# Kernel optimization log

Measured on AMD Instinct MI355X. Metric: run time of the kernel, lower is better.

## Reference

```python
import jax, jax.numpy as jnp
import numpy as np

N, E, G, F = 50000, 800000, 64, 128
R_MAX = 5.0
P_CUT = 6.0
NUM_BESSEL = 8


def sph_harm(u):
    # component-normalized real spherical harmonics up to l=3 on unit vectors u [E,3]
    x, y, z = u[:, 0], u[:, 1], u[:, 2]
    one = jnp.ones_like(x)
    s3, s5, s15 = np.sqrt(3.0), np.sqrt(5.0), np.sqrt(15.0)
    c1, c2, c3 = np.sqrt(35.0 / 8.0), np.sqrt(105.0), np.sqrt(21.0 / 8.0)
    c4, c5 = np.sqrt(7.0) / 2.0, np.sqrt(105.0) / 2.0
    x2, y2, z2 = x * x, y * y, z * z
    comps = [
        one,
        s3 * x, s3 * y, s3 * z,
        s15 * x * y, s15 * y * z, 0.5 * s5 * (3.0 * z2 - 1.0), s15 * x * z, 0.5 * s15 * (x2 - y2),
        c1 * y * (3.0 * x2 - y2), c2 * x * y * z, c3 * y * (5.0 * z2 - 1.0),
        c4 * z * (5.0 * z2 - 3.0), c3 * x * (5.0 * z2 - 1.0), c5 * z * (x2 - y2),
        c1 * x * (x2 - 3.0 * y2),
    ]
    return jnp.stack(comps, axis=-1)  # [E,16]


def radial_embedding(r):
    # Bessel basis with polynomial cutoff envelope; r [E]
    n = jnp.arange(1, NUM_BESSEL + 1, dtype=r.dtype)
    bessel = np.sqrt(2.0 / R_MAX) * jnp.sin(n * jnp.pi * r[:, None] / R_MAX) / r[:, None]
    u = r / R_MAX
    p = P_CUT
    env = (1.0 - (p + 1.0) * (p + 2.0) / 2.0 * u ** p
           + p * (p + 2.0) * u ** (p + 1.0)
           - p * (p + 1.0) / 2.0 * u ** (p + 2.0))
    env = env * (r < R_MAX).astype(r.dtype)
    return bessel * env[:, None]  # [E,8]


def setup_inputs() -> dict:
    key = jax.random.key(0)
    ks = jax.random.split(key, 12)
    return {
        "positions": jax.random.normal(ks[0], (N, 3), dtype=jnp.float32),
        "node_attrs": jax.random.uniform(ks[1], (N, 10), dtype=jnp.float32),
        "shifts": jnp.zeros((E, 3), dtype=jnp.float32),
        "edge_index": jax.random.randint(ks[2], (2, E), 0, N),
        "batch": jnp.sort(jax.random.randint(ks[3], (N,), 0, G)),
        "num_graphs": G,
        "W_emb": 0.1 * jax.random.normal(ks[4], (10, F), dtype=jnp.float32),
        "atomic_energies_t": jax.random.normal(ks[5], (10,), dtype=jnp.float32),
        "W_r": 0.1 * jax.random.normal(ks[6], (2, NUM_BESSEL, F), dtype=jnp.float32),
        "w_sh": 0.1 * jax.random.normal(ks[7], (2, 16), dtype=jnp.float32),
        "W_out": 0.1 * jax.random.normal(ks[8], (2, F, F), dtype=jnp.float32),
        "W_skip": 0.1 * jax.random.normal(ks[9], (2, 10, F), dtype=jnp.float32),
        "w_read": 0.1 * jax.random.normal(ks[10], (2, F), dtype=jnp.float32),
    }


def reference(positions, node_attrs, shifts, edge_index, batch, num_graphs,
              W_emb, atomic_energies_t, W_r, w_sh, W_out, W_skip, w_read):
    snd, rcv = edge_index[0], edge_index[1]

    def energy_fn(pos):
        vec = pos[rcv] - pos[snd] + shifts                      # [E,3] edge gather
        r = jnp.sqrt(jnp.sum(vec * vec, axis=-1) + 1e-12)       # [E]
        Y = sph_harm(vec / r[:, None])                          # [E,16]
        eb = radial_embedding(r)                                # [E,8]
        h = node_attrs @ W_emb                                  # [N,F] node embedding
        e0 = jax.ops.segment_sum(node_attrs @ atomic_energies_t, batch, num_segments=num_graphs)
        energy = e0
        for i in range(W_r.shape[0]):                           # interaction layers
            R = eb @ W_r[i]                                     # [E,F] radial weights
            s = Y @ w_sh[i]                                     # [E] angular weight
            m = h[snd] * R * s[:, None]                         # [E,F] messages
            agg = jax.ops.segment_sum(m, rcv, num_segments=pos.shape[0])  # [N,F]
            h = agg @ W_out[i] + node_attrs @ W_skip[i]
            node_e = h @ w_read[i]                              # [N] readout
            energy = energy + jax.ops.segment_sum(node_e, batch, num_segments=num_graphs)
        return energy                                           # [G]

    energy = energy_fn(positions)
    forces = -jax.grad(lambda p: energy_fn(p).sum())(positions)
    return energy, forces
```

## Files before the change

kernel.cpp:

```cpp
#include <hip/hip_runtime.h>

#define NN 50000
#define EE 800000
#define GG 64
#define FF 128
#define NBES 8
#define RECW 8
#define RMAXF 5.0f
#define PI_F 3.14159265358979323846f
#define NB ((NN + 255) / 256)

#define S3  1.7320508075688772f
#define S5  2.23606797749979f
#define S15 3.872983346207417f
#define C1c 2.091650066335189f
#define C2c 10.246950765959598f
#define C3c 1.62018517460196f
#define C4c 1.3228756555322954f
#define C5c 5.123475382979799f
#define CCB 0.6324555320336759f

__device__ __forceinline__ float shc_s(float x, float y, float z, const float* __restrict__ w) {
    float x2 = x * x, y2 = y * y, z2 = z * z;
    return w[0]
        + w[1] * (S3 * x) + w[2] * (S3 * y) + w[3] * (S3 * z)
        + w[4] * (S15 * x * y) + w[5] * (S15 * y * z) + w[6] * (0.5f * S5 * (3.f * z2 - 1.f))
        + w[7] * (S15 * x * z) + w[8] * (0.5f * S15 * (x2 - y2))
        + w[9] * (C1c * y * (3.f * x2 - y2)) + w[10] * (C2c * x * y * z)
        + w[11] * (C3c * y * (5.f * z2 - 1.f)) + w[12] * (C4c * z * (5.f * z2 - 3.f))
        + w[13] * (C3c * x * (5.f * z2 - 1.f)) + w[14] * (C5c * z * (x2 - y2))
        + w[15] * (C1c * x * (x2 - 3.f * y2));
}

__device__ __forceinline__ void shc_grad(float x, float y, float z, const float* __restrict__ w,
                                         float& gx, float& gy, float& gz) {
    float x2 = x * x, y2 = y * y, z2 = z * z;
    gx = w[1] * S3 + w[4] * (S15 * y) + w[7] * (S15 * z) + w[8] * (S15 * x)
       + w[9] * (6.f * C1c * x * y) + w[10] * (C2c * y * z) + w[13] * (C3c * (5.f * z2 - 1.f))
       + w[14] * (2.f * C5c * x * z) + w[15] * (3.f * C1c * (x2 - y2));
    gy = w[2] * S3 + w[4] * (S15 * x) + w[5] * (S15 * z) - w[8] * (S15 * y)
       + w[9] * (3.f * C1c * (x2 - y2)) + w[10] * (C2c * x * z) + w[11] * (C3c * (5.f * z2 - 1.f))
       - w[14] * (2.f * C5c * y * z) - w[15] * (6.f * C1c * x * y);
    gz = w[3] * S3 + w[5] * (S15 * y) + w[6] * (3.f * S5 * z) + w[7] * (S15 * x)
       + w[10] * (C2c * x * y) + w[11] * (10.f * C3c * y * z) + w[12] * (C4c * (15.f * z2 - 3.f))
       + w[13] * (10.f * C3c * x * z) + w[14] * (C5c * (x2 - y2));
}


__global__ __launch_bounds__(256) void count_kernel(const int* __restrict__ ei,
                                                    int* __restrict__ cnt,
                                                    int* __restrict__ rank_r,
                                                    int* __restrict__ rank_s) {
    int e = blockIdx.x * 256 + threadIdx.x;
    if (e >= EE) return;
    rank_r[e] = atomicAdd(&cnt[ei[EE + e]], 1);
    rank_s[e] = atomicAdd(&cnt[NN + ei[e]], 1);
}

__global__ __launch_bounds__(256) void scan_partial(const int* __restrict__ cnt,
                                                    int* __restrict__ parts) {
    __shared__ int wsum[4];
    int b = blockIdx.x;
    int half = b / NB;
    int cb = b - half * NB;
    int i = cb * 256 + threadIdx.x;
    int v = (i < NN) ? cnt[(size_t)half * NN + i] : 0;
    int x = v;
#pragma unroll
    for (int o = 32; o > 0; o >>= 1) x += __shfl_xor(x, o);
    int lane = threadIdx.x & 63, wid = threadIdx.x >> 6;
    if (lane == 0) wsum[wid] = x;
    __syncthreads();
    if (threadIdx.x == 0) parts[b] = wsum[0] + wsum[1] + wsum[2] + wsum[3];
}

__global__ __launch_bounds__(256) void scan_parts(int* __restrict__ parts,
                                                  int* __restrict__ off) {
    __shared__ int wsum[4];
    __shared__ int carry_s;
    int lane = threadIdx.x & 63, wid = threadIdx.x >> 6;
    for (int h = 0; h < 2; h++) {
        if (threadIdx.x == 0) carry_s = 0;
        __syncthreads();
        for (int base = 0; base < NB; base += 256) {
            int i = base + threadIdx.x;
            int v = (i < NB) ? parts[h * NB + i] : 0;
            int x = v;
#pragma unroll
            for (int d = 1; d < 64; d <<= 1) {
                int y = __shfl_up(x, d);
                if (lane >= d) x += y;
            }
            if (lane == 63) wsum[wid] = x;
            __syncthreads();
            int pre = 0;
#pragma unroll
            for (int w = 0; w < 4; w++) if (w < wid) pre += wsum[w];
            int total = wsum[0] + wsum[1] + wsum[2] + wsum[3];
            int carry = carry_s;
            if (i < NB) parts[h * NB + i] = carry + pre + x - v;
            __syncthreads();
            if (threadIdx.x == 0) carry_s = carry + total;
            __syncthreads();
        }
        if (threadIdx.x == 0) off[(size_t)h * (NN + 1) + NN] = carry_s;
        __syncthreads();
    }
}

__global__ __launch_bounds__(256) void scan_apply(const int* __restrict__ cnt,
                                                  const int* __restrict__ parts,
                                                  int* __restrict__ off) {
    __shared__ int wsum[4];
    int b = blockIdx.x;
    int half = b / NB;
    int cb = b - half * NB;
    int i = cb * 256 + threadIdx.x;
    int v = (i < NN) ? cnt[(size_t)half * NN + i] : 0;
    int lane = threadIdx.x & 63, wid = threadIdx.x >> 6;
    int x = v;
#pragma unroll
    for (int d = 1; d < 64; d <<= 1) {
        int y = __shfl_up(x, d);
        if (lane >= d) x += y;
    }
    if (lane == 63) wsum[wid] = x;
    __syncthreads();
    int pre = 0;
#pragma unroll
    for (int w = 0; w < 4; w++) if (w < wid) pre += wsum[w];
    if (i < NN) off[(size_t)half * (NN + 1) + i] = parts[b] + pre + x - v;
}

__global__ __launch_bounds__(256) void fill_kernel(const int* __restrict__ ei,
                                                   const int* __restrict__ off,
                                                   const int* __restrict__ rank_r,
                                                   const int* __restrict__ rank_s,
                                                   int* __restrict__ jr,
                                                   int* __restrict__ psl_j) {
    int e = blockIdx.x * 256 + threadIdx.x;
    if (e >= EE) return;
    int snd = ei[e], rcv = ei[EE + e];
    int sr = off[rcv] + rank_r[e];
    int ss = off[(NN + 1) + snd] + rank_s[e];
    jr[e] = sr;
    psl_j[ss] = sr;
}


__global__ __launch_bounds__(256) void edge_geom(const float* __restrict__ pos,
                                                 const float* __restrict__ shifts,
                                                 const int* __restrict__ ei,
                                                 const float* __restrict__ wsh,
                                                 const int* __restrict__ jr,
                                                 float* __restrict__ rec) {
    int e = blockIdx.x * 256 + threadIdx.x;
    if (e >= EE) return;
    int snd = ei[e];
    int rcv = ei[EE + e];
    float vx = pos[rcv * 3 + 0] - pos[snd * 3 + 0] + shifts[e * 3 + 0];
    float vy = pos[rcv * 3 + 1] - pos[snd * 3 + 1] + shifts[e * 3 + 1];
    float vz = pos[rcv * 3 + 2] - pos[snd * 3 + 2] + shifts[e * 3 + 2];
    float r2 = vx * vx + vy * vy + vz * vz + 1e-12f;
    float r = sqrtf(r2);
    float inv_r = 1.0f / r;
    float x = vx * inv_r, y = vy * inv_r, z = vz * inv_r;

    float s0 = shc_s(x, y, z, wsh);
    float s1v = shc_s(x, y, z, wsh + 16);

    float* rc = rec + (size_t)jr[e] * RECW;
    *(float4*)&rc[0] = make_float4(x, y, z, inv_r);
    *(float4*)&rc[4] = make_float4(s0, s1v, __int_as_float(snd), __int_as_float(rcv));
}


__global__ __launch_bounds__(256) void e1_csr(const float* __restrict__ rec,
                                              const int* __restrict__ off_snd,
                                              const int* __restrict__ psl_j,
                                              float* __restrict__ E1) {
    int gid = blockIdx.x * 256 + threadIdx.x;
    int n = gid >> 3;
    int k_l = gid & 7;
    if (n >= NN) return;
    float kf = (float)(k_l + 1);
    int beg = off_snd[n], end = off_snd[n + 1];
    float acc = 0.f;
    for (int s = beg; s < end; s++) {
        int j = psl_j[s];
        const float* rc = rec + (size_t)j * RECW;
        float inv_r = rc[3];
        float s1v = rc[5];
        float r = 1.0f / inv_r;
        float u = r * (1.0f / RMAXF);
        float th = PI_F * u;
        float u2 = u * u, u3 = u2 * u, u6 = u3 * u3, u7 = u6 * u, u8 = u6 * u2;
        float valid = (r < RMAXF) ? 1.f : 0.f;
        float env = (1.f - 28.f * u6 + 48.f * u7 - 21.f * u8) * valid;
        float my = sinf(kf * th);
        acc += my * (CCB * inv_r * env * s1v);
    }
    E1[(size_t)n * 8 + k_l] = acc;
}


__global__ __launch_bounds__(128) void a1_kernel(const float* __restrict__ Wout1,
                                                 const float* __restrict__ wread1,
                                                 const float* __restrict__ Wskip1,
                                                 const float* __restrict__ ae,
                                                 float* __restrict__ a1,
                                                 float* __restrict__ askip) {
    int f = threadIdx.x;
    float s = 0.f;
    for (int k = 0; k < FF; k++) s += Wout1[f * FF + k] * wread1[k];
    a1[f] = s;
    if (f < 10) {
        float t = 0.f;
        for (int k = 0; k < FF; k++) t += Wskip1[f * FF + k] * wread1[k];
        askip[f] = t + ae[f];
    }
}

__global__ __launch_bounds__(128) void cd_kernel(const float* __restrict__ Wout0,
                                                 const float* __restrict__ wread0,
                                                 const float* __restrict__ a1,
                                                 const float* __restrict__ Wr1,
                                                 float* __restrict__ c0,
                                                 float* __restrict__ D) {
    int fp = threadIdx.x;
    float c = 0.f;
    float d[NBES];
#pragma unroll
    for (int k = 0; k < NBES; k++) d[k] = 0.f;
    for (int f = 0; f < FF; f++) {
        float w = Wout0[fp * FF + f];
        c += wread0[f] * w;
        float aw = a1[f] * w;
#pragma unroll
        for (int k = 0; k < NBES; k++) d[k] += aw * Wr1[k * FF + f];
    }
    c0[fp] = c;
#pragma unroll
    for (int k = 0; k < NBES; k++) D[k * FF + fp] = d[k];
}

__global__ __launch_bounds__(256) void gw_kernel(const float* __restrict__ W_emb,
                                                 const float* __restrict__ Wr0,
                                                 const float* __restrict__ Wout0,
                                                 float* __restrict__ GW) {
    int idx = blockIdx.x * 256 + threadIdx.x;
    if (idx >= 80 * FF) return;
    int fp = idx & 127;
    int p = idx >> 7;
    int a = p >> 3, k = p & 7;
    float s = 0.f;
    for (int f = 0; f < FF; f++)
        s += W_emb[a * FF + f] * Wr0[k * FF + f] * Wout0[f * FF + fp];
    GW[p * FF + fp] = s;
}

__global__ __launch_bounds__(256) void tmc_kernel(const float* __restrict__ D,
                                                  const float* __restrict__ c0,
                                                  const float* __restrict__ W_emb,
                                                  const float* __restrict__ Wr0,
                                                  float* __restrict__ T,
                                                  float* __restrict__ Mc) {
    for (int i = threadIdx.x; i < 720; i += 256) {
        if (i < 640) {
            int kp = i / 80;
            int p0 = i - kp * 80;
            int k = p0 / 10, a = p0 - k * 10;
            float s = 0.f;
            for (int f = 0; f < FF; f++)
                s += D[kp * FF + f] * W_emb[a * FF + f] * Wr0[k * FF + f];
            T[i] = s;
        } else {
            int p0 = i - 640;
            int k = p0 / 10, a = p0 - k * 10;
            float s = 0.f;
            for (int f = 0; f < FF; f++)
                s += c0[f] * W_emb[a * FF + f] * Wr0[k * FF + f];
            Mc[p0] = s;
        }
    }
}


#define P0_BLOCKS 2048
__global__ __launch_bounds__(256) void p0_kernel(const float* __restrict__ rec,
                                                 const int* __restrict__ off,
                                                 const float* __restrict__ attrs,
                                                 float* __restrict__ P0) {
    int wv = (blockIdx.x * 256 + threadIdx.x) >> 6;
    int lane = threadIdx.x & 63;
    int nwaves = P0_BLOCKS * 4;
    int a_lo = lane >> 3;
    int k_l = lane & 7;
    float kf = (float)(k_l + 1);

    for (int n = wv; n < NN; n += nwaves) {
        int beg = off[n], end = off[n + 1];
        float acc = 0.f, acc2 = 0.f;
        for (int j = beg; j < end; j++) {
            const float* rc = rec + (size_t)j * RECW;
            float inv_r = rc[3];
            float s0 = rc[4];
            int snd = __float_as_int(rc[6]);
            float r = 1.0f / inv_r;
            float u = r * (1.0f / RMAXF);
            float th = PI_F * u;
            float u2 = u * u, u3 = u2 * u, u6 = u3 * u3, u7 = u6 * u, u8 = u6 * u2;
            float valid = (r < RMAXF) ? 1.f : 0.f;
            float env = (1.f - 28.f * u6 + 48.f * u7 - 21.f * u8) * valid;
            float my = sinf(kf * th);
            float es = my * (CCB * inv_r * env) * s0;
            acc += attrs[snd * 10 + a_lo] * es;
            if (lane < 16) acc2 += attrs[snd * 10 + 8 + a_lo] * es;
        }
        P0[(size_t)n * 80 + lane] = acc;
        if (lane < 16) P0[(size_t)n * 80 + 64 + lane] = acc2;
    }
}


#define GEMM_BLOCKS 512
__global__ __launch_bounds__(256, 2) void h1_gemm(const float* __restrict__ P0,
                                                  const float* __restrict__ GW,
                                                  const float* __restrict__ attrs,
                                                  const float* __restrict__ Wskip,
                                                  const float* __restrict__ wread,
                                                  float* __restrict__ h1,
                                                  float* __restrict__ node_e) {
    __shared__ float sb[80][FF];
    __shared__ float sa[32][80];
    int t = threadIdx.x;
#pragma unroll
    for (int j = 0; j < 10; j++) {
        int flat4 = j * 256 + t;
        int row = flat4 >> 5;
        int col = (flat4 & 31) * 4;
        *(float4*)&sb[row][col] = *(const float4*)&GW[row * FF + col];
    }

    int g = t >> 5;
    int f0 = (t & 31) * 4;
    const int NTILES = (NN + 31) / 32;

    for (int tile = blockIdx.x; tile < NTILES; tile += GEMM_BLOCKS) {
        __syncthreads();
#pragma unroll
        for (int j = 0; j < 3; j++) {
            int flat4 = j * 256 + t;
            if (flat4 < 640) {
                int row = flat4 / 20;
                int col = (flat4 - row * 20) * 4;
                int n = tile * 32 + row;
                float4 v = make_float4(0.f, 0.f, 0.f, 0.f);
                if (n < NN) v = *(const float4*)&P0[(size_t)n * 80 + col];
                *(float4*)&sa[row][col] = v;
            }
        }
        __syncthreads();

        float acc[4][4];
#pragma unroll
        for (int i = 0; i < 4; i++)
#pragma unroll
            for (int j = 0; j < 4; j++) acc[i][j] = 0.f;

        for (int kk = 0; kk < 80; kk += 4) {
            float4 bv0 = *(const float4*)&sb[kk + 0][f0];
            float4 bv1 = *(const float4*)&sb[kk + 1][f0];
            float4 bv2 = *(const float4*)&sb[kk + 2][f0];
            float4 bv3 = *(const float4*)&sb[kk + 3][f0];
#pragma unroll
            for (int ni = 0; ni < 4; ni++) {
                float4 av = *(const float4*)&sa[g * 4 + ni][kk];
                acc[ni][0] += av.x * bv0.x + av.y * bv1.x + av.z * bv2.x + av.w * bv3.x;
                acc[ni][1] += av.x * bv0.y + av.y * bv1.y + av.z * bv2.y + av.w * bv3.y;
                acc[ni][2] += av.x * bv0.z + av.y * bv1.z + av.z * bv2.z + av.w * bv3.z;
                acc[ni][3] += av.x * bv0.w + av.y * bv1.w + av.z * bv2.w + av.w * bv3.w;
            }
        }

#pragma unroll
        for (int ni = 0; ni < 4; ni++) {
            int n = tile * 32 + g * 4 + ni;
            bool valid = (n < NN);
#pragma unroll
            for (int a = 0; a < 10; a++) {
                float att = valid ? attrs[n * 10 + a] : 0.f;
                float4 wk = *(const float4*)&Wskip[a * FF + f0];
                acc[ni][0] += att * wk.x;
                acc[ni][1] += att * wk.y;
                acc[ni][2] += att * wk.z;
                acc[ni][3] += att * wk.w;
            }
            if (valid) {
                float4 out;
                out.x = acc[ni][0]; out.y = acc[ni][1];
                out.z = acc[ni][2]; out.w = acc[ni][3];
                *(float4*)&h1[(size_t)n * FF + f0] = out;
            }
            float4 wv = *(const float4*)&wread[f0];
            float p = acc[ni][0] * wv.x + acc[ni][1] * wv.y
                    + acc[ni][2] * wv.z + acc[ni][3] * wv.w;
#pragma unroll
            for (int o = 16; o > 0; o >>= 1) p += __shfl_xor(p, o);
            if (valid && (t & 31) == 0) node_e[n] = p;
        }
    }
}


__global__ __launch_bounds__(256) void t1_kernel(const float* __restrict__ h1,
                                                 const float* __restrict__ a1,
                                                 const float* __restrict__ Wr1,
                                                 float* __restrict__ t1) {
    int w = threadIdx.x >> 6;
    int lane = threadIdx.x & 63;
    int n = blockIdx.x * 4 + w;
    if (n >= NN) return;
    int f0 = lane, f1 = lane + 64;
    float v0 = a1[f0] * h1[(size_t)n * FF + f0];
    float v1 = a1[f1] * h1[(size_t)n * FF + f1];
    float p[NBES];
#pragma unroll
    for (int k = 0; k < NBES; k++)
        p[k] = v0 * Wr1[k * FF + f0] + v1 * Wr1[k * FF + f1];
#pragma unroll
    for (int o = 32; o > 0; o >>= 1) {
#pragma unroll
        for (int k = 0; k < NBES; k++) p[k] += __shfl_xor(p[k], o);
    }
    if (lane == 0) {
        *(float4*)&t1[(size_t)n * 8]     = make_float4(p[0], p[1], p[2], p[3]);
        *(float4*)&t1[(size_t)n * 8 + 4] = make_float4(p[4], p[5], p[6], p[7]);
    }
}


__global__ __launch_bounds__(256) void m_kernel(const float* __restrict__ E1,
                                                const float* __restrict__ T,
                                                const float* __restrict__ Mc,
                                                float* __restrict__ M) {
    __shared__ float sT[720];
    int t = threadIdx.x;
    for (int i = t; i < 720; i += 256) sT[i] = (i < 640) ? T[i] : Mc[i - 640];
    __syncthreads();
    int n = blockIdx.x * 256 + t;
    if (n >= NN) return;
    float4 ea = *(const float4*)&E1[(size_t)n * 8];
    float4 eb = *(const float4*)&E1[(size_t)n * 8 + 4];
    float e1v[8] = {ea.x, ea.y, ea.z, ea.w, eb.x, eb.y, eb.z, eb.w};
#pragma unroll
    for (int c = 0; c < 20; c++) {
        float4 m = *(const float4*)&sT[640 + c * 4];
#pragma unroll
        for (int kp = 0; kp < 8; kp++) {
            float4 tv = *(const float4*)&sT[kp * 80 + c * 4];
            m.x += e1v[kp] * tv.x;
            m.y += e1v[kp] * tv.y;
            m.z += e1v[kp] * tv.z;
            m.w += e1v[kp] * tv.w;
        }
        *(float4*)&M[(size_t)n * 80 + c * 4] = m;
    }
}


#define EP_BLOCKS 512
__global__ __launch_bounds__(256) void edge_pass(const float* __restrict__ rec,
                                                 const float* __restrict__ t1,
                                                 const float* __restrict__ M,
                                                 const float* __restrict__ attrs,
                                                 const int* __restrict__ batch,
                                                 const float* __restrict__ wsh,
                                                 float4* __restrict__ gvp,
                                                 float* __restrict__ energy) {
    __shared__ float eacc[GG];
    int t = threadIdx.x;
    int lane = t & 63;
    if (t < GG) eacc[t] = 0.f;
    __syncthreads();

    for (int j0 = blockIdx.x * 256; j0 < EE; j0 += EP_BLOCKS * 256) {
        int j = j0 + t;
        bool act = (j < EE);
        int jc = act ? j : 0;
        const float* rc = rec + (size_t)jc * RECW;
        float4 q0 = *(const float4*)&rc[0];
        float4 q1 = *(const float4*)&rc[4];
        float x = q0.x, y = q0.y, z = q0.z, ivr = q0.w;
        float s0 = q1.x, s1v = q1.y;
        int snd = __float_as_int(q1.z);
        int rcv = __float_as_int(q1.w);

        float r = 1.0f / ivr;
        float u = r * (1.0f / RMAXF);
        float th = PI_F * u;
        float s1 = sinf(th), c1 = cosf(th);
        float u2 = u * u, u3 = u2 * u, u5 = u2 * u3, u6 = u3 * u3, u7 = u6 * u, u8 = u6 * u2;
        float valid = (r < RMAXF) ? 1.f : 0.f;
        float env = (1.f - 28.f * u6 + 48.f * u7 - 21.f * u8) * valid;
        float denv = (-168.f * u5 + 336.f * u6 - 168.f * u7) * (1.0f / RMAXF) * valid;
        float eb[NBES], db[NBES];
        {
            float sk = s1, skm = 0.f, ck = c1, ckm = 1.f;
            float tc = 2.f * c1;
#pragma unroll
            for (int k = 1; k <= NBES; k++) {
                float b = CCB * sk * ivr;
                eb[k - 1] = b * env;
                db[k - 1] = CCB * (((float)k * PI_F * (1.0f / RMAXF)) * ck * ivr
                                   - sk * ivr * ivr) * env
                            + b * denv;
                float sn = tc * sk - skm; skm = sk; sk = sn;
                float cn = tc * ck - ckm; ckm = ck; ck = cn;
            }
        }

        float4 ta = *(const float4*)&t1[(size_t)snd * 8];
        float4 tb = *(const float4*)&t1[(size_t)snd * 8 + 4];
        float tg[8] = {ta.x, ta.y, ta.z, ta.w, tb.x, tb.y, tb.z, tb.w};
        float dsp1 = 0.f, drp1 = 0.f;
#pragma unroll
        for (int k = 0; k < 8; k++) {
            dsp1 += eb[k] * tg[k];
            drp1 += db[k] * tg[k];
        }

        float at[10];
#pragma unroll
        for (int i = 0; i < 5; i++) {
            float2 v = *(const float2*)&attrs[snd * 10 + 2 * i];
            at[2 * i] = v.x; at[2 * i + 1] = v.y;
        }
        const float* Mr = M + (size_t)rcv * 80;
        float dsp0 = 0.f, drp0 = 0.f;
#pragma unroll
        for (int k = 0; k < 8; k++) {
            float t0 = 0.f;
#pragma unroll
            for (int a = 0; a < 10; a++) t0 += at[a] * Mr[k * 10 + a];
            dsp0 += eb[k] * t0;
            drp0 += db[k] * t0;
        }

        float el = act ? s1v * dsp1 : 0.f;
        int b = act ? batch[rcv] : -1;
        int ub = __builtin_amdgcn_readfirstlane(b);
        if (__all(b == ub)) {
            float es = el;
#pragma unroll
            for (int o = 32; o > 0; o >>= 1) es += __shfl_xor(es, o);
            if (lane == 0 && ub >= 0) atomicAdd(&eacc[ub], es);
        } else {
            if (act) atomicAdd(&eacc[b], el);
        }

        float g0x, g0y, g0z, g1x, g1y, g1z;
        shc_grad(x, y, z, wsh, g0x, g0y, g0z);
        shc_grad(x, y, z, wsh + 16, g1x, g1y, g1z);
        float gux = dsp0 * g0x + dsp1 * g1x;
        float guy = dsp0 * g0y + dsp1 * g1y;
        float guz = dsp0 * g0z + dsp1 * g1z;
        float gr = s0 * drp0 + s1v * drp1;
        float dgu = gux * x + guy * y + guz * z;
        float gvx = gr * x + ivr * (gux - dgu * x);
        float gvy = gr * y + ivr * (guy - dgu * y);
        float gvz = gr * z + ivr * (guz - dgu * z);
        if (act) gvp[j] = make_float4(gvx, gvy, gvz, 0.f);
    }
    __syncthreads();
    if (t < GG && eacc[t] != 0.f) atomicAdd(&energy[t], eacc[t]);
}


__global__ __launch_bounds__(256) void force_gather(const int* __restrict__ off_rcv,
                                                    const int* __restrict__ off_snd,
                                                    const int* __restrict__ psl_j,
                                                    const float4* __restrict__ gvp,
                                                    float* __restrict__ forces) {
    int n = blockIdx.x * 256 + threadIdx.x;
    if (n >= NN) return;
    float fx = 0.f, fy = 0.f, fz = 0.f;
    int beg = off_rcv[n], end = off_rcv[n + 1];
    for (int j = beg; j < end; j++) {
        float4 g = gvp[j];
        fx -= g.x; fy -= g.y; fz -= g.z;
    }
    beg = off_snd[n]; end = off_snd[n + 1];
    for (int s = beg; s < end; s++) {
        float4 g = gvp[psl_j[s]];
        fx += g.x; fy += g.y; fz += g.z;
    }
    forces[n * 3 + 0] = fx;
    forces[n * 3 + 1] = fy;
    forces[n * 3 + 2] = fz;
}


#define EF_BLOCKS 128
__global__ __launch_bounds__(256) void efinal_kernel(const float* __restrict__ node_e,
                                                     const float* __restrict__ attrs,
                                                     const float* __restrict__ askip,
                                                     const int* __restrict__ batch,
                                                     float* __restrict__ energy) {
    __shared__ float eacc[GG];
    int t = threadIdx.x;
    if (t < GG) eacc[t] = 0.f;
    __syncthreads();
    for (int n = blockIdx.x * 256 + t; n < NN; n += EF_BLOCKS * 256) {
        float v = node_e[n];
#pragma unroll
        for (int a = 0; a < 10; a++) v += attrs[n * 10 + a] * askip[a];
        atomicAdd(&eacc[batch[n]], v);
    }
    __syncthreads();
    if (t < GG && eacc[t] != 0.f) atomicAdd(&energy[t], eacc[t]);
}


extern "C" void kernel_launch(void* const* d_in, const int* in_sizes, int n_in,
                              void* d_out, int out_size, void* d_ws, size_t ws_size,
                              hipStream_t stream) {
    const float* pos    = (const float*)d_in[0];
    const float* attrs  = (const float*)d_in[1];
    const float* shifts = (const float*)d_in[2];
    const int*   ei     = (const int*)d_in[3];
    const int*   batch  = (const int*)d_in[4];
    const float* W_emb  = (const float*)d_in[6];
    const float* ae     = (const float*)d_in[7];
    const float* W_r    = (const float*)d_in[8];
    const float* w_sh   = (const float*)d_in[9];
    const float* W_out  = (const float*)d_in[10];
    const float* W_skip = (const float*)d_in[11];
    const float* w_read = (const float*)d_in[12];

    const float* Wr0 = W_r;
    const float* Wr1 = W_r + NBES * FF;
    const float* Wout0 = W_out;
    const float* Wout1 = W_out + FF * FF;

    float* energy = (float*)d_out;
    float* forces = energy + GG;

    float* ws  = (float*)d_ws;
    float* h1  = ws;
    float* P0  = h1 + (size_t)NN * FF;
    float* M   = P0 + (size_t)NN * 80;
    float* E1  = M + (size_t)NN * 80;
    float* t1  = E1 + (size_t)NN * 8;
    float* node_e = t1 + (size_t)NN * 8;
    float* rec = node_e + NN;
    float4* gvp = (float4*)(rec + (size_t)EE * RECW);
    float* a1  = (float*)(gvp + EE);
    float* askip = a1 + FF;
    float* c0  = askip + 16;
    float* D   = c0 + FF;
    float* GW  = D + NBES * FF;
    float* T   = GW + 80 * FF;
    float* Mc  = T + 640;

    int* cnt    = (int*)(Mc + 80);
    int* off    = cnt + 2 * NN;
    int* rank_r = off + 2 * (NN + 1);
    int* rank_s = rank_r + EE;
    int* jr     = rank_s + EE;
    int* psl_j  = jr + EE;
    int* parts  = psl_j + EE;
    const int* off_rcv = off;
    const int* off_snd = off + (NN + 1);

    const int edgeBlocks = (EE + 255) / 256;
    const int nodeBlocks = (NN + 255) / 256;

    hipMemsetAsync(d_out, 0, (size_t)out_size * sizeof(float), stream);
    hipMemsetAsync(cnt, 0, (size_t)2 * NN * sizeof(int), stream);

    count_kernel<<<edgeBlocks, 256, 0, stream>>>(ei, cnt, rank_r, rank_s);
    scan_partial<<<2 * NB, 256, 0, stream>>>(cnt, parts);
    scan_parts<<<1, 256, 0, stream>>>(parts, off);
    scan_apply<<<2 * NB, 256, 0, stream>>>(cnt, parts, off);
    fill_kernel<<<edgeBlocks, 256, 0, stream>>>(ei, off, rank_r, rank_s, jr, psl_j);

    a1_kernel<<<1, 128, 0, stream>>>(Wout1, w_read + FF, W_skip + 10 * FF, ae, a1, askip);
    cd_kernel<<<1, 128, 0, stream>>>(Wout0, w_read, a1, Wr1, c0, D);
    gw_kernel<<<40, 256, 0, stream>>>(W_emb, Wr0, Wout0, GW);
    tmc_kernel<<<1, 256, 0, stream>>>(D, c0, W_emb, Wr0, T, Mc);

    edge_geom<<<edgeBlocks, 256, 0, stream>>>(pos, shifts, ei, w_sh, jr, rec);

    e1_csr<<<(NN * 8 + 255) / 256, 256, 0, stream>>>(rec, off_snd, psl_j, E1);

    p0_kernel<<<P0_BLOCKS, 256, 0, stream>>>(rec, off_rcv, attrs, P0);
    h1_gemm<<<GEMM_BLOCKS, 256, 0, stream>>>(P0, GW, attrs, W_skip, w_read, h1, node_e);
    t1_kernel<<<(NN + 3) / 4, 256, 0, stream>>>(h1, a1, Wr1, t1);
    m_kernel<<<nodeBlocks, 256, 0, stream>>>(E1, T, Mc, M);

    edge_pass<<<EP_BLOCKS, 256, 0, stream>>>(rec, t1, M, attrs, batch, w_sh, gvp, energy);

    force_gather<<<nodeBlocks, 256, 0, stream>>>(off_rcv, off_snd, psl_j, gvp, forces);

    efinal_kernel<<<EF_BLOCKS, 256, 0, stream>>>(node_e, attrs, askip, batch, energy);
}
```

Before: 412.8 us.

## Precompute per-edge Bessel-envelope products once in edge_geom, stored in CSR orders

edge_geom now computes the 8 radial Bessel values once per edge, using a sin/cos recurrence instead of 8 separate sinf calls. It multiplies them by each layer's angular weight and writes two 8-float arrays: one in receiver-CSR order and one in sender-CSR order. e1_csr and p0_kernel then stream these precomputed values instead of recomputing the envelope and sinf for every (edge, k) pair. The cost is about 51 MB of extra writes and reads plus an extra index array, traded against the redundant transcendental work.

```diff
diff --git a/kernel.cpp b/kernel.cpp
--- a/kernel.cpp
+++ b/kernel.cpp
@@ -137,6 +137,7 @@
                                                    const int* __restrict__ rank_r,
                                                    const int* __restrict__ rank_s,
                                                    int* __restrict__ jr,
+                                                   int* __restrict__ js,
                                                    int* __restrict__ psl_j) {
     int e = blockIdx.x * 256 + threadIdx.x;
     if (e >= EE) return;
@@ -144,6 +145,7 @@
     int sr = off[rcv] + rank_r[e];
     int ss = off[(NN + 1) + snd] + rank_s[e];
     jr[e] = sr;
+    js[e] = ss;
     psl_j[ss] = sr;
 }
 
@@ -153,7 +155,10 @@
                                                  const int* __restrict__ ei,
                                                  const float* __restrict__ wsh,
                                                  const int* __restrict__ jr,
-                                                 float* __restrict__ rec) {
+                                                 const int* __restrict__ js,
+                                                 float* __restrict__ rec,
+                                                 float* __restrict__ ebs0,
+                                                 float* __restrict__ ebs1) {
     int e = blockIdx.x * 256 + threadIdx.x;
     if (e >= EE) return;
     int snd = ei[e];
@@ -172,34 +177,43 @@
     float* rc = rec + (size_t)jr[e] * RECW;
     *(float4*)&rc[0] = make_float4(x, y, z, inv_r);
     *(float4*)&rc[4] = make_float4(s0, s1v, __int_as_float(snd), __int_as_float(rcv));
-}
-
-
-__global__ __launch_bounds__(256) void e1_csr(const float* __restrict__ rec,
+
+    float u = r * (1.0f / RMAXF);
+    float th = PI_F * u;
+    float s1 = sinf(th), c1 = cosf(th);
+    float u2 = u * u, u3 = u2 * u, u6 = u3 * u3, u7 = u6 * u, u8 = u6 * u2;
+    float valid = (r < RMAXF) ? 1.f : 0.f;
+    float env = (1.f - 28.f * u6 + 48.f * u7 - 21.f * u8) * valid;
+    float base = CCB * inv_r * env;
+    float ebv[NBES];
+    {
+        float sk = s1, skm = 0.f;
+        float tc = 2.f * c1;
+#pragma unroll
+        for (int k = 0; k < NBES; k++) {
+            ebv[k] = sk * base;
+            float sn = tc * sk - skm; skm = sk; sk = sn;
+        }
+    }
+    float* p0p = ebs0 + (size_t)jr[e] * 8;
+    *(float4*)&p0p[0] = make_float4(ebv[0] * s0, ebv[1] * s0, ebv[2] * s0, ebv[3] * s0);
+    *(float4*)&p0p[4] = make_float4(ebv[4] * s0, ebv[5] * s0, ebv[6] * s0, ebv[7] * s0);
+    float* p1p = ebs1 + (size_t)js[e] * 8;
+    *(float4*)&p1p[0] = make_float4(ebv[0] * s1v, ebv[1] * s1v, ebv[2] * s1v, ebv[3] * s1v);
+    *(float4*)&p1p[4] = make_float4(ebv[4] * s1v, ebv[5] * s1v, ebv[6] * s1v, ebv[7] * s1v);
+}
+
+
+__global__ __launch_bounds__(256) void e1_csr(const float* __restrict__ ebs1,
                                               const int* __restrict__ off_snd,
-                                              const int* __restrict__ psl_j,
                                               float* __restrict__ E1) {
     int gid = blockIdx.x * 256 + threadIdx.x;
     int n = gid >> 3;
     int k_l = gid & 7;
     if (n >= NN) return;
-    float kf = (float)(k_l + 1);
     int beg = off_snd[n], end = off_snd[n + 1];
     float acc = 0.f;
-    for (int s = beg; s < end; s++) {
-        int j = psl_j[s];
-        const float* rc = rec + (size_t)j * RECW;
-        float inv_r = rc[3];
-        float s1v = rc[5];
-        float r = 1.0f / inv_r;
-        float u = r * (1.0f / RMAXF);
-        float th = PI_F * u;
-        float u2 = u * u, u3 = u2 * u, u6 = u3 * u3, u7 = u6 * u, u8 = u6 * u2;
-        float valid = (r < RMAXF) ? 1.f : 0.f;
-        float env = (1.f - 28.f * u6 + 48.f * u7 - 21.f * u8) * valid;
-        float my = sinf(kf * th);
-        acc += my * (CCB * inv_r * env * s1v);
-    }
+    for (int s = beg; s < end; s++) acc += ebs1[(size_t)s * 8 + k_l];
     E1[(size_t)n * 8 + k_l] = acc;
 }
 
@@ -288,6 +302,7 @@
 
 #define P0_BLOCKS 2048
 __global__ __launch_bounds__(256) void p0_kernel(const float* __restrict__ rec,
+                                                 const float* __restrict__ ebs0,
                                                  const int* __restrict__ off,
                                                  const float* __restrict__ attrs,
                                                  float* __restrict__ P0) {
@@ -296,24 +311,13 @@
     int nwaves = P0_BLOCKS * 4;
     int a_lo = lane >> 3;
     int k_l = lane & 7;
-    float kf = (float)(k_l + 1);
 
     for (int n = wv; n < NN; n += nwaves) {
         int beg = off[n], end = off[n + 1];
         float acc = 0.f, acc2 = 0.f;
         for (int j = beg; j < end; j++) {
-            const float* rc = rec + (size_t)j * RECW;
-            float inv_r = rc[3];
-            float s0 = rc[4];
-            int snd = __float_as_int(rc[6]);
-            float r = 1.0f / inv_r;
-            float u = r * (1.0f / RMAXF);
-            float th = PI_F * u;
-            float u2 = u * u, u3 = u2 * u, u6 = u3 * u3, u7 = u6 * u, u8 = u6 * u2;
-            float valid = (r < RMAXF) ? 1.f : 0.f;
-            float env = (1.f - 28.f * u6 + 48.f * u7 - 21.f * u8) * valid;
-            float my = sinf(kf * th);
-            float es = my * (CCB * inv_r * env) * s0;
+            float es = ebs0[(size_t)j * 8 + k_l];
+            int snd = __float_as_int(rec[(size_t)j * RECW + 6]);
             acc += attrs[snd * 10 + a_lo] * es;
             if (lane < 16) acc2 += attrs[snd * 10 + 8 + a_lo] * es;
         }
@@ -654,7 +658,9 @@
     float* t1  = E1 + (size_t)NN * 8;
     float* node_e = t1 + (size_t)NN * 8;
     float* rec = node_e + NN;
-    float4* gvp = (float4*)(rec + (size_t)EE * RECW);
+    float* ebs0 = rec + (size_t)EE * RECW;
+    float* ebs1 = ebs0 + (size_t)EE * 8;
+    float4* gvp = (float4*)(ebs1 + (size_t)EE * 8);
     float* a1  = (float*)(gvp + EE);
     float* askip = a1 + FF;
     float* c0  = askip + 16;
@@ -668,7 +674,8 @@
     int* rank_r = off + 2 * (NN + 1);
     int* rank_s = rank_r + EE;
     int* jr     = rank_s + EE;
-    int* psl_j  = jr + EE;
+    int* js     = jr + EE;
+    int* psl_j  = js + EE;
     int* parts  = psl_j + EE;
     const int* off_rcv = off;
     const int* off_snd = off + (NN + 1);
@@ -683,18 +690,19 @@
     scan_partial<<<2 * NB, 256, 0, stream>>>(cnt, parts);
     scan_parts<<<1, 256, 0, stream>>>(parts, off);
     scan_apply<<<2 * NB, 256, 0, stream>>>(cnt, parts, off);
-    fill_kernel<<<edgeBlocks, 256, 0, stream>>>(ei, off, rank_r, rank_s, jr, psl_j);
+    fill_kernel<<<edgeBlocks, 256, 0, stream>>>(ei, off, rank_r, rank_s, jr, js, psl_j);
 
     a1_kernel<<<1, 128, 0, stream>>>(Wout1, w_read + FF, W_skip + 10 * FF, ae, a1, askip);
     cd_kernel<<<1, 128, 0, stream>>>(Wout0, w_read, a1, Wr1, c0, D);
     gw_kernel<<<40, 256, 0, stream>>>(W_emb, Wr0, Wout0, GW);
     tmc_kernel<<<1, 256, 0, stream>>>(D, c0, W_emb, Wr0, T, Mc);
 
-    edge_geom<<<edgeBlocks, 256, 0, stream>>>(pos, shifts, ei, w_sh, jr, rec);
-
-    e1_csr<<<(NN * 8 + 255) / 256, 256, 0, stream>>>(rec, off_snd, psl_j, E1);
-
-    p0_kernel<<<P0_BLOCKS, 256, 0, stream>>>(rec, off_rcv, attrs, P0);
+    edge_geom<<<edgeBlocks, 256, 0, stream>>>(pos, shifts, ei, w_sh, jr, js,
+                                              rec, ebs0, ebs1);
+
+    e1_csr<<<(NN * 8 + 255) / 256, 256, 0, stream>>>(ebs1, off_snd, E1);
+
+    p0_kernel<<<P0_BLOCKS, 256, 0, stream>>>(rec, ebs0, off_rcv, attrs, P0);
     h1_gemm<<<GEMM_BLOCKS, 256, 0, stream>>>(P0, GW, attrs, W_skip, w_read, h1, node_e);
     t1_kernel<<<(NN + 3) / 4, 256, 0, stream>>>(h1, a1, Wr1, t1);
     m_kernel<<<nodeBlocks, 256, 0, stream>>>(E1, T, Mc, M);
```

Measured after the change: 402.4 us. -2.5%, faster.
